# Performance work log

Hardware: AMD Instinct MI355X
Metric: run time of the kernel (lower is better)

The kernel has to match this reference:

```python
import jax, jax.numpy as jnp
import numpy as np

B, L, H, E = 16, 4096, 8, 64
K = 64  # topk modes
SCALE = 1.0 / (512 * 512)  # 1/(in_channels*out_channels)


def setup_inputs() -> dict:
    key = jax.random.key(0)
    k1, k2, k3 = jax.random.split(key, 3)
    q = jax.random.normal(k1, (B, L, H, E), dtype=jnp.float32)
    k = jnp.zeros((B, L, H, E), jnp.float32)  # unused by module
    v = jnp.zeros((B, L, H, E), jnp.float32)  # unused by module
    mask = jnp.zeros((1,), jnp.int32)         # unused by module
    w_real = jax.random.uniform(k2, (K, H, E, E), dtype=jnp.float32) * SCALE
    w_imag = jax.random.uniform(k3, (K, H, E, E), dtype=jnp.float32) * SCALE
    return {"q": q, "k": k, "v": v, "w_real": w_real, "w_imag": w_imag, "mask": mask}


def reference(q, k, v, w_real, w_imag, mask):
    # x_ft: (B, F, H, Ein) complex64, F = L//2 + 1
    x_ft = jnp.fft.rfft(q.astype(jnp.float32), axis=1)
    F = x_ft.shape[1]
    kk = w_real.shape[0]
    # energy score per bin: sum |.|^2 over Ein, mean over batch, mean over heads
    e = (x_ft.real ** 2 + x_ft.imag ** 2).sum(-1)      # (B, F, H)
    score = e.mean(0).mean(-1)                          # (F,)
    score = score.at[0].set(-jnp.inf)                   # topk_exclude_dc=True
    _, idx = jax.lax.top_k(score, kk)                   # sorted desc by energy
    # gather selected modes: (B, K, H, Ein)
    x_sel = x_ft[:, idx]
    w = jax.lax.complex(w_real, w_imag)                 # (K, H, Ein, Eout)
    out_sel = jnp.einsum('bkhe,khef->bkhf', x_sel, w)   # per-head complex matmul
    # packed scatter: selected modes written into the first K bins of zero spectrum
    out_ft = jnp.zeros((x_ft.shape[0], F, x_ft.shape[2], w.shape[-1]), jnp.complex64)
    out_ft = out_ft.at[:, :kk].set(out_sel)
    # inverse FFT back to time domain, norm='backward' (default)
    return jnp.fft.irfft(out_ft, n=q.shape[1], axis=1)
```

## Files before the change

### kernel.cpp

```cpp
#include <hip/hip_runtime.h>
#include <hip/hip_fp16.h>


#define NTHREADS 256

typedef _Float16 f16x8 __attribute__((ext_vector_type(8)));
typedef float    f32x4 __attribute__((ext_vector_type(4)));

__device__ inline void lds_barrier() {
    asm volatile("s_waitcnt lgkmcnt(0)" ::: "memory");
    __builtin_amdgcn_s_barrier();
}

#define ZI(i) ((i) ^ ((((i) >> 4) & 7) << 1))

__device__ inline float2 f2add(float2 a, float2 b) { return make_float2(a.x + b.x, a.y + b.y); }
__device__ inline float2 f2sub(float2 a, float2 b) { return make_float2(a.x - b.x, a.y - b.y); }
__device__ inline float2 cmulf(float2 a, float2 b) {
    return make_float2(__builtin_fmaf(a.x, b.x, -(a.y * b.y)),
                       __builtin_fmaf(a.x, b.y,  a.y * b.x));
}

__device__ inline void radix16(float2 x[16], float2 tA, float2 tB, float2 tC, float2 tD) {
#pragma unroll
    for (int q = 0; q < 8; ++q) {
        float2 v = cmulf(tA, x[2 * q + 1]);
        float2 u = x[2 * q];
        x[2 * q]     = f2add(u, v);
        x[2 * q + 1] = f2sub(u, v);
    }
    {
        float2 tB1 = make_float2(tB.y, -tB.x);
#pragma unroll
        for (int q = 0; q < 4; ++q) {
            {
                float2 v = cmulf(tB, x[4 * q + 2]);
                float2 u = x[4 * q];
                x[4 * q]     = f2add(u, v);
                x[4 * q + 2] = f2sub(u, v);
            }
            {
                float2 v = cmulf(tB1, x[4 * q + 3]);
                float2 u = x[4 * q + 1];
                x[4 * q + 1] = f2add(u, v);
                x[4 * q + 3] = f2sub(u, v);
            }
        }
    }
    {
        const float C = 0.70710678118654752f;
        float2 w0 = tC;
        float2 w1 = cmulf(tC, make_float2(C, -C));
        float2 w2 = make_float2(tC.y, -tC.x);
        float2 w3 = cmulf(tC, make_float2(-C, -C));
#pragma unroll
        for (int q = 0; q < 2; ++q) {
            float2 ws[4] = {w0, w1, w2, w3};
#pragma unroll
            for (int r = 0; r < 4; ++r) {
                float2 v = cmulf(ws[r], x[8 * q + r + 4]);
                float2 u = x[8 * q + r];
                x[8 * q + r]     = f2add(u, v);
                x[8 * q + r + 4] = f2sub(u, v);
            }
        }
    }
    {
        const float C  = 0.70710678118654752f;
        const float C1 = 0.92387953251128676f;
        const float S1 = 0.38268343236508977f;
        float2 wD[8];
        wD[0] = tD;
        wD[1] = cmulf(tD, make_float2(C1, -S1));
        wD[2] = cmulf(tD, make_float2(C, -C));
        wD[3] = cmulf(tD, make_float2(S1, -C1));
        wD[4] = make_float2(tD.y, -tD.x);
        wD[5] = cmulf(tD, make_float2(-S1, -C1));
        wD[6] = cmulf(tD, make_float2(-C, -C));
        wD[7] = cmulf(tD, make_float2(-C1, -S1));
#pragma unroll
        for (int r = 0; r < 8; ++r) {
            float2 v = cmulf(wD[r], x[r + 8]);
            float2 u = x[r];
            x[r]     = f2add(u, v);
            x[r + 8] = f2sub(u, v);
        }
    }
}

__global__ __launch_bounds__(256) void k_init(float2* __restrict__ trig,
                                              unsigned long long* __restrict__ score,
                                              _Float16* __restrict__ Af) {
    const int g = blockIdx.x * 256 + threadIdx.x;
    if (g < 4096) {
        double th = (6.283185307179586476925286766559 * (double)g) / 4096.0;
        trig[g] = make_float2((float)cos(th), (float)sin(th));
        if (g < 2048) score[g] = 0ULL;
    } else {
        const int gid = g - 4096;
        const int l = gid >> 7, k = gid & 127;
        const int kk = (k < 64) ? k : k - 64;
        const int ph = (kk * l) & 4095;
        const float th = 1.5339807878856412e-3f * (float)ph;
        float v = (k < 64) ? __cosf(th) : -__sinf(th);
        Af[gid] = (_Float16)v;
    }
}

__global__ __launch_bounds__(256) void k_xpose(const float* __restrict__ q,
                                               float2* __restrict__ T) {
    __shared__ float tile[128][65];

    const int tid = threadIdx.x;
    const int bi  = blockIdx.x;
    const int b   = bi >> 8;
    const int h   = (bi >> 5) & 7;
    const int c5  = bi & 31;

    const float* qb = q + ((size_t)b * 4096 * 512) + (size_t)h * 64;
#pragma unroll
    for (int i = 0; i < 8; ++i) {
        const int f = tid + 256 * i;
        const int t = f >> 4, e4 = f & 15;
        const float4 v = *(const float4*)(qb + (size_t)(c5 + 32 * t) * 512 + e4 * 4);
        tile[t][e4 * 4 + 0] = v.x;
        tile[t][e4 * 4 + 1] = v.y;
        tile[t][e4 * 4 + 2] = v.z;
        tile[t][e4 * 4 + 3] = v.w;
    }
    lds_barrier();

    const int wave = tid >> 6, lane = tid & 63;
    const int rl  = __brev(lane) >> 26;
    const int r5c = __brev(c5) >> 27;
    for (int cc = wave; cc < 32; cc += 4) {
        const int eo = cc >> 2, p = cc & 3;
        const int col0 = eo * 8 + 2 * p;
        float2* dst = T + ((size_t)((b * 8 + h) * 8 + eo)) * 16384 + (size_t)p * 4096
                        + (size_t)r5c * 128;
        float4 o;
        o.x = tile[rl][col0];      o.y = tile[rl][col0 + 1];
        o.z = tile[rl + 64][col0]; o.w = tile[rl + 64][col0 + 1];
        *(float4*)(dst + 2 * lane) = o;
    }
}

__global__ __launch_bounds__(256) void k_fft(const float2* __restrict__ trig,
                                             float2* __restrict__ Xout,
                                             unsigned long long* __restrict__ score) {
    __shared__ float2 z[4096];
    __shared__ float2 ctw4[80];

    const int tid = threadIdx.x;
    const int bi  = blockIdx.x;

    if (tid < 64) {
        const int j = tid >> 2, qq = tid & 3;
        float2 a = trig[j << (7 - qq)];
        ctw4[5 * j + qq] = make_float2(a.x, -a.y);
    }

    float eaccr[8];
#pragma unroll
    for (int k = 0; k < 8; ++k) eaccr[k] = 0.f;

    const float2 ONE = make_float2(1.0f, 0.0f);
    const float2* base = Xout + (size_t)bi * 16384;
    __half2* Xh = (__half2*)Xout;

    float4 pre[8];
#pragma unroll
    for (int g = 0; g < 8; ++g) pre[g] = *(const float4*)(base + 16 * tid + 2 * g);
    lds_barrier();

    for (int p = 0; p < 4; ++p) {
        float2 x[16];
#pragma unroll
        for (int g = 0; g < 8; ++g) {
            x[2 * g]     = make_float2(pre[g].x, pre[g].y);
            x[2 * g + 1] = make_float2(pre[g].z, pre[g].w);
        }
        if (p < 3) {
            const float2* pn = base + (size_t)(p + 1) * 4096;
#pragma unroll
            for (int g = 0; g < 8; ++g) pre[g] = *(const float4*)(pn + 16 * tid + 2 * g);
        }

        radix16(x, ONE, ONE, ONE, ONE);
        {
            const int i0 = 16 * tid;
#pragma unroll
            for (int s = 0; s < 8; ++s) {
                *(float4*)&z[ZI(i0 + 2 * s)] = make_float4(x[2 * s].x, x[2 * s].y,
                                                           x[2 * s + 1].x, x[2 * s + 1].y);
            }
        }
        lds_barrier();

        {
            const int j = tid & 15;
            const int g = tid >> 4;
            const int i0 = (g << 8) + j;
            int ad[16];
#pragma unroll
            for (int k = 0; k < 16; ++k) ad[k] = ZI(i0 + 16 * k);
#pragma unroll
            for (int k = 0; k < 16; ++k) x[k] = z[ad[k]];
            const float2 tA = ctw4[5 * j + 0];
            const float2 tB = ctw4[5 * j + 1];
            const float2 tC = ctw4[5 * j + 2];
            const float2 tD = ctw4[5 * j + 3];
            radix16(x, tA, tB, tC, tD);
#pragma unroll
            for (int k = 0; k < 16; ++k) z[ad[k]] = x[k];
        }
        lds_barrier();

        {
            const int j = tid;
            int ad[16];
#pragma unroll
            for (int k = 0; k < 16; ++k) ad[k] = ZI(j + 256 * k);
#pragma unroll
            for (int k = 0; k < 16; ++k) x[k] = z[ad[k]];
            float2 a = trig[j << 3], b2 = trig[j << 2], c = trig[j << 1], d = trig[j];
            const float2 tA = make_float2(a.x, -a.y);
            const float2 tB = make_float2(b2.x, -b2.y);
            const float2 tC = make_float2(c.x, -c.y);
            const float2 tD = make_float2(d.x, -d.y);
            radix16(x, tA, tB, tC, tD);
#pragma unroll
            for (int k = 0; k < 16; ++k) z[ad[k]] = x[k];
        }
        lds_barrier();

        {
            const size_t s0 = (size_t)bi * 32768 + (size_t)p * 4096;
#pragma unroll
            for (int k = 0; k < 8; ++k) {
                const int t = tid + 256 * k;
                const int m = t + 1;
                float2 Za = z[ZI(m)];
                float2 Zb = z[ZI(4096 - m)];
                float Xr0 = 0.5f * (Za.x + Zb.x);
                float Xi0 = 0.5f * (Za.y - Zb.y);
                float Xr1 = 0.5f * (Za.y + Zb.y);
                float Xi1 = 0.5f * (Zb.x - Za.x);
                Xh[s0 + t]        = __floats2half2_rn(Xr0, Xi0);
                Xh[s0 + 2048 + t] = __floats2half2_rn(Xr1, Xi1);
                eaccr[k] += Xr0 * Xr0 + Xi0 * Xi0 + Xr1 * Xr1 + Xi1 * Xi1;
            }
        }
        lds_barrier();
    }

#pragma unroll
    for (int k = 0; k < 8; ++k) {
        unsigned long long v = (unsigned long long)llrintf(eaccr[k] * 1048576.0f);
        atomicAdd(&score[tid + 256 * k], v);
    }
}

__global__ __launch_bounds__(256) void k_topk(const unsigned long long* __restrict__ score,
                                              int* __restrict__ idx) {
    __shared__ unsigned long long s[2048];
    const int tid = threadIdx.x;
    for (int t = tid; t < 2048; t += 256) s[t] = score[t];
    __syncthreads();

    const int t = blockIdx.x * 256 + tid;
    const unsigned long long my = s[t];
    int rank = 0;
#pragma unroll 8
    for (int u = 0; u < 2048; ++u) {
        unsigned long long o = s[u];
        rank += (int)((o > my) || (o == my && u < t));
    }
    if (rank < 64) idx[rank] = t + 1;
}

__global__ __launch_bounds__(256) void k_proj(const __half2* __restrict__ Xh,
                                              const float* __restrict__ wr,
                                              const float* __restrict__ wi,
                                              const int* __restrict__ idx,
                                              _Float16* __restrict__ Yt) {
    __shared__ __align__(16) float2 xs[4 * 64];
    __shared__ float  wrs[64 * 64];
    __shared__ float  wis[64 * 64];

    const int tid = threadIdx.x;
    const int j  = blockIdx.x >> 5;
    const int h  = (blockIdx.x >> 2) & 7;
    const int bq = blockIdx.x & 3;
    const int m = idx[j];

    {
        const int bl = tid >> 6, e = tid & 63;
        const int sig = (((bq * 4 + bl) * 8 + h) * 64 + e);
        const size_t xi = (size_t)(sig >> 3) * 32768 + (size_t)((sig >> 1) & 3) * 4096
                        + (size_t)(sig & 1) * 2048 + (size_t)(m - 1);
        xs[tid] = __half22float2(Xh[xi]);
    }
    const float* wrb = wr + ((size_t)(j * 8 + h)) * 4096;
    const float* wib = wi + ((size_t)(j * 8 + h)) * 4096;
#pragma unroll
    for (int i = 0; i < 16; ++i) {
        const int t = tid + 256 * i;
        wrs[t] = wrb[t];
        wis[t] = wib[t];
    }
    lds_barrier();

    const int bl = tid >> 6;
    const int f  = tid & 63;
    const float2* xrow = &xs[bl * 64];
    float yr = 0.f, yi = 0.f;
#pragma unroll
    for (int e = 0; e < 64; e += 4) {
        const float4 xa = *(const float4*)&xrow[e];
        const float4 xb = *(const float4*)&xrow[e + 2];
        const float2 xv[4] = {make_float2(xa.x, xa.y), make_float2(xa.z, xa.w),
                              make_float2(xb.x, xb.y), make_float2(xb.z, xb.w)};
#pragma unroll
        for (int d = 0; d < 4; ++d) {
            const float a = wrs[(e + d) * 64 + f], cc = wis[(e + d) * 64 + f];
            yr = __builtin_fmaf(xv[d].x, a, yr); yr = __builtin_fmaf(-xv[d].y, cc, yr);
            yi = __builtin_fmaf(xv[d].x, cc, yi); yi = __builtin_fmaf( xv[d].y, a, yi);
        }
    }
    const int b  = bq * 4 + bl;
    const int hf = h * 64 + f;
    _Float16* yt = Yt + ((size_t)b * 512 + (size_t)hf) * 128;
    yt[j]      = (_Float16)(j == 0 ? 0.5f * yr : yr);
    yt[64 + j] = (_Float16)yi;
}

__global__ __launch_bounds__(256) void k_synth(const _Float16* __restrict__ Af,
                                               const _Float16* __restrict__ Yt,
                                               float* __restrict__ out) {
    const int tid  = threadIdx.x;
    const int wv   = tid >> 6;
    const int lane = tid & 63;
    const int bi   = blockIdx.x;
    const int b    = bi >> 8;
    const int ng   = (bi >> 6) & 3;
    const int lt   = bi & 63;

    const int l0 = lt * 64;
    const int n0 = ng * 128 + wv * 32;

    const int row = lane & 15;
    const int kb  = lane >> 4;

    f32x4 acc[4][2] = {};

    const _Float16* Ab = Af + (size_t)l0 * 128;
    const _Float16* Bb = Yt + (size_t)b * 512 * 128 + (size_t)n0 * 128;

#pragma unroll
    for (int k0 = 0; k0 < 128; k0 += 32) {
        f16x8 a[4], bf[2];
#pragma unroll
        for (int mt = 0; mt < 4; ++mt)
            a[mt] = *(const f16x8*)(Ab + (size_t)(mt * 16 + row) * 128 + k0 + kb * 8);
#pragma unroll
        for (int nt = 0; nt < 2; ++nt)
            bf[nt] = *(const f16x8*)(Bb + (size_t)(nt * 16 + row) * 128 + k0 + kb * 8);
#pragma unroll
        for (int mt = 0; mt < 4; ++mt)
#pragma unroll
            for (int nt = 0; nt < 2; ++nt)
                acc[mt][nt] = __builtin_amdgcn_mfma_f32_16x16x32_f16(a[mt], bf[nt],
                                                                     acc[mt][nt], 0, 0, 0);
    }

    const float s = 2.0f / 4096.0f;
#pragma unroll
    for (int mt = 0; mt < 4; ++mt) {
#pragma unroll
        for (int nt = 0; nt < 2; ++nt) {
            const int col = n0 + nt * 16 + row;
#pragma unroll
            for (int r = 0; r < 4; ++r) {
                const int mrow = mt * 16 + kb * 4 + r;
                out[((size_t)(b * 4096 + l0 + mrow)) * 512 + col] = acc[mt][nt][r] * s;
            }
        }
    }
}

extern "C" void kernel_launch(void* const* d_in, const int* in_sizes, int n_in,
                              void* d_out, int out_size, void* d_ws, size_t ws_size,
                              hipStream_t stream) {
    const float* q  = (const float*)d_in[0];
    const float* wr = (const float*)d_in[3];
    const float* wi = (const float*)d_in[4];

    char* ws = (char*)d_ws;
    float2*             trig  = (float2*)(ws + 0);
    unsigned long long* score = (unsigned long long*)(ws + 32768);
    int*                idx   = (int*)(ws + 49152);
    _Float16*           Af    = (_Float16*)(ws + 65536);
    _Float16*           Yt    = (_Float16*)(ws + 65536 + 1048576);

    float2* Xs = (float2*)d_out;

    k_init<<<2064, 256, 0, stream>>>(trig, score, Af);
    k_xpose<<<4096, 256, 0, stream>>>(q, Xs);
    k_fft<<<1024, 256, 0, stream>>>(trig, Xs, score);
    k_topk<<<8, 256, 0, stream>>>(score, idx);
    k_proj<<<2048, 256, 0, stream>>>((const __half2*)Xs, wr, wi, idx, Yt);
    k_synth<<<4096, 256, 0, stream>>>(Af, Yt, (float*)d_out);
}
```

Measured before the change: 228.7 us.

## Split FFT blocks in half and keep twiddles in registers

The FFT kernel now launches twice as many blocks, each handling two of the four signal pairs instead of all four, with the output layout adjusted accordingly in the projection kernel's indexing. Twiddle factors for both radix-16 passes are loaded once into registers up front, replacing the shared-memory twiddle table and the per-iteration global twiddle loads. This aims to improve occupancy and latency hiding on the GPU at the cost of more register pressure and duplicated twiddle/prefetch setup per block; the score accumulation tail (not shown) must remain correct under the split.

After: 242.6 us. 6.0% more time.

```diff
diff --git a/kernel.cpp b/kernel.cpp
--- a/kernel.cpp
+++ b/kernel.cpp
@@ -149,15 +149,22 @@
                                              float2* __restrict__ Xout,
                                              unsigned long long* __restrict__ score) {
     __shared__ float2 z[4096];
-    __shared__ float2 ctw4[80];
 
     const int tid = threadIdx.x;
-    const int bi  = blockIdx.x;
-
-    if (tid < 64) {
-        const int j = tid >> 2, qq = tid & 3;
-        float2 a = trig[j << (7 - qq)];
-        ctw4[5 * j + qq] = make_float2(a.x, -a.y);
+    const int bi  = blockIdx.x >> 1;
+    const int hh  = blockIdx.x & 1;
+
+    const int j1 = tid & 15;
+    float2 p1A, p1B, p1C, p1D, p2A, p2B, p2C, p2D;
+    {
+        float2 a = trig[j1 << 7], b = trig[j1 << 6], c = trig[j1 << 5], d = trig[j1 << 4];
+        p1A = make_float2(a.x, -a.y); p1B = make_float2(b.x, -b.y);
+        p1C = make_float2(c.x, -c.y); p1D = make_float2(d.x, -d.y);
+    }
+    {
+        float2 a = trig[tid << 3], b = trig[tid << 2], c = trig[tid << 1], d = trig[tid];
+        p2A = make_float2(a.x, -a.y); p2B = make_float2(b.x, -b.y);
+        p2C = make_float2(c.x, -c.y); p2D = make_float2(d.x, -d.y);
     }
 
     float eaccr[8];
@@ -165,23 +172,23 @@
     for (int k = 0; k < 8; ++k) eaccr[k] = 0.f;
 
     const float2 ONE = make_float2(1.0f, 0.0f);
-    const float2* base = Xout + (size_t)bi * 16384;
+    const float2* base = Xout + (size_t)bi * 16384 + (size_t)hh * 8192;
     __half2* Xh = (__half2*)Xout;
 
     float4 pre[8];
 #pragma unroll
     for (int g = 0; g < 8; ++g) pre[g] = *(const float4*)(base + 16 * tid + 2 * g);
-    lds_barrier();
-
-    for (int p = 0; p < 4; ++p) {
+
+#pragma unroll
+    for (int pl = 0; pl < 2; ++pl) {
         float2 x[16];
 #pragma unroll
         for (int g = 0; g < 8; ++g) {
             x[2 * g]     = make_float2(pre[g].x, pre[g].y);
             x[2 * g + 1] = make_float2(pre[g].z, pre[g].w);
         }
-        if (p < 3) {
-            const float2* pn = base + (size_t)(p + 1) * 4096;
+        if (pl == 0) {
+            const float2* pn = base + 4096;
 #pragma unroll
             for (int g = 0; g < 8; ++g) pre[g] = *(const float4*)(pn + 16 * tid + 2 * g);
         }
@@ -198,44 +205,33 @@
         lds_barrier();
 
         {
-            const int j = tid & 15;
             const int g = tid >> 4;
-            const int i0 = (g << 8) + j;
+            const int i0 = (g << 8) + j1;
             int ad[16];
 #pragma unroll
             for (int k = 0; k < 16; ++k) ad[k] = ZI(i0 + 16 * k);
 #pragma unroll
             for (int k = 0; k < 16; ++k) x[k] = z[ad[k]];
-            const float2 tA = ctw4[5 * j + 0];
-            const float2 tB = ctw4[5 * j + 1];
-            const float2 tC = ctw4[5 * j + 2];
-            const float2 tD = ctw4[5 * j + 3];
-            radix16(x, tA, tB, tC, tD);
+            radix16(x, p1A, p1B, p1C, p1D);
 #pragma unroll
             for (int k = 0; k < 16; ++k) z[ad[k]] = x[k];
         }
         lds_barrier();
 
         {
-            const int j = tid;
             int ad[16];
 #pragma unroll
-            for (int k = 0; k < 16; ++k) ad[k] = ZI(j + 256 * k);
+            for (int k = 0; k < 16; ++k) ad[k] = ZI(tid + 256 * k);
 #pragma unroll
             for (int k = 0; k < 16; ++k) x[k] = z[ad[k]];
-            float2 a = trig[j << 3], b2 = trig[j << 2], c = trig[j << 1], d = trig[j];
-            const float2 tA = make_float2(a.x, -a.y);
-            const float2 tB = make_float2(b2.x, -b2.y);
-            const float2 tC = make_float2(c.x, -c.y);
-            const float2 tD = make_float2(d.x, -d.y);
-            radix16(x, tA, tB, tC, tD);
+            radix16(x, p2A, p2B, p2C, p2D);
 #pragma unroll
             for (int k = 0; k < 16; ++k) z[ad[k]] = x[k];
         }
         lds_barrier();
 
         {
-            const size_t s0 = (size_t)bi * 32768 + (size_t)p * 4096;
+            const size_t s0 = (size_t)bi * 32768 + (size_t)hh * 8192 + (size_t)pl * 4096;
 #pragma unroll
             for (int k = 0; k < 8; ++k) {
                 const int t = tid + 256 * k;
@@ -297,8 +293,9 @@
     {
         const int bl = tid >> 6, e = tid & 63;
         const int sig = (((bq * 4 + bl) * 8 + h) * 64 + e);
-        const size_t xi = (size_t)(sig >> 3) * 32768 + (size_t)((sig >> 1) & 3) * 4096
-                        + (size_t)(sig & 1) * 2048 + (size_t)(m - 1);
+        const int p2 = (sig >> 1) & 3;
+        const size_t xi = (size_t)(sig >> 3) * 32768 + (size_t)(p2 >> 1) * 8192
+                        + (size_t)(p2 & 1) * 4096 + (size_t)(sig & 1) * 2048 + (size_t)(m - 1);
         xs[tid] = __half22float2(Xh[xi]);
     }
     const float* wrb = wr + ((size_t)(j * 8 + h)) * 4096;
@@ -407,7 +404,7 @@
 
     k_init<<<2064, 256, 0, stream>>>(trig, score, Af);
     k_xpose<<<4096, 256, 0, stream>>>(q, Xs);
-    k_fft<<<1024, 256, 0, stream>>>(trig, Xs, score);
+    k_fft<<<2048, 256, 0, stream>>>(trig, Xs, score);
     k_topk<<<8, 256, 0, stream>>>(score, idx);
     k_proj<<<2048, 256, 0, stream>>>((const __half2*)Xs, wr, wi, idx, Yt);
     k_synth<<<4096, 256, 0, stream>>>(Af, Yt, (float*)d_out);
```
